# Kernel tuning notes

Hardware: AMD Instinct MI355X
Metric: run time of the kernel (lower is better)

## Reference

```python
import jax, jax.numpy as jnp
import numpy as np
from jax import lax

N = 20000        # nodes
E = 320000       # directed edges (avg degree 16)
F_IN = 512       # input feature dim
HID = 64         # hidden_layer
K_NEI = 8        # sampled neighbors per node
L = K_NEI + 1    # local subgraph size (self + neighbors)
N_TPL = 10       # N_templates
NT = 8           # N_templates_nodes
N_CLS = 6
ALPHA = 0.5      # FGW trade-off
EPS = 0.1        # entropic regularization
N_OUTER = 3      # outer CG iterations
N_SINK = 5       # sinkhorn iterations per outer step


def setup_inputs() -> dict:
    rng = np.random.default_rng(0)
    src = rng.integers(0, N, E).astype(np.int64)
    dst = rng.integers(0, N, E).astype(np.int64)
    edge_index = np.stack([src, dst])

    # fixed-size neighbor table (pad with self, mask)
    nbr = np.full((N, K_NEI), -1, np.int64)
    cnt = np.zeros(N, np.int64)
    for s, d in zip(src, dst):
        c = cnt[s]
        if c < K_NEI:
            nbr[s, c] = d
            cnt[s] = c + 1
    pad = nbr < 0
    self_col = np.arange(N, dtype=np.int64)
    nbr = np.where(pad, self_col[:, None], nbr)
    nbr_mask = np.concatenate([np.ones((N, 1)), (~pad).astype(np.float64)], 1).astype(np.float32)

    # local adjacency among {self, neighbors}: [N, L, L]
    idx_full = np.concatenate([self_col[:, None], nbr], 1)  # [N, L]
    edge_keys = np.unique(src * N + dst)
    keys = idx_full[:, :, None] * N + idx_full[:, None, :]
    C_local = np.isin(keys, edge_keys).astype(np.float32)

    ks = jax.random.split(jax.random.key(0), 10)
    x = jax.random.normal(ks[0], (N, F_IN), jnp.float32)
    W1 = jax.random.normal(ks[1], (F_IN, HID), jnp.float32) / np.float32(np.sqrt(F_IN))
    b1 = jnp.zeros((HID,), jnp.float32)
    W2 = jax.random.normal(ks[2], (HID, HID), jnp.float32) / np.float32(np.sqrt(HID))
    b2 = jnp.zeros((HID,), jnp.float32)
    t = jax.random.uniform(ks[3], (N_TPL, NT, NT), jnp.float32)
    templates = 0.5 * (t + jnp.swapaxes(t, 1, 2))  # symmetric template adjacency
    templates_features = jax.random.normal(ks[4], (N_TPL, NT, HID), jnp.float32)
    Wlin = jax.random.normal(ks[5], (HID + N_TPL, N_CLS), jnp.float32) / np.float32(np.sqrt(HID + N_TPL))
    blin = jnp.zeros((N_CLS,), jnp.float32)
    return {"x": x, "edge_index": jnp.asarray(edge_index), "nbr_idx": jnp.asarray(nbr),
            "nbr_mask": jnp.asarray(nbr_mask), "C_local": jnp.asarray(C_local),
            "W1": W1, "b1": b1, "W2": W2, "b2": b2,
            "templates": templates, "templates_features": templates_features,
            "Wlin": Wlin, "blin": blin}


def gcn(x, W, b, src, dst, n):
    xw = x @ W
    sl = jnp.arange(n)
    s = jnp.concatenate([src, sl])
    d = jnp.concatenate([dst, sl])
    deg = jax.ops.segment_sum(jnp.ones_like(s, jnp.float32), d, num_segments=n)
    dinv = lax.rsqrt(deg)
    coef = dinv[s] * dinv[d]
    return jax.ops.segment_sum(xw[s] * coef[:, None], d, num_segments=n) + b


def fgw_dist(M, C1, h1, C2, h2):
    # entropic fused GW (square loss) with fixed iterations; padded rows have h1 = 0
    f1 = C1 * C1
    f2 = C2 * C2
    constC = (f1 @ h1)[:, None] + (f2 @ h2)[None, :]
    T0 = h1[:, None] * h2[None, :]

    def outer(T, _):
        tens = constC - 2.0 * (C1 @ T @ C2)
        G = (1.0 - ALPHA) * M + ALPHA * tens
        Kmat = jnp.exp(-G / EPS)

        def sink(carry, _):
            u, v = carry
            u = h1 / (Kmat @ v + 1e-16)
            v = h2 / (Kmat.T @ u + 1e-16)
            return (u, v), None

        (u, v), _ = lax.scan(sink, (jnp.ones_like(h1), jnp.ones_like(h2)), None, length=N_SINK)
        return u[:, None] * Kmat * v[None, :], None

    T, _ = lax.scan(outer, T0, None, length=N_OUTER)
    tens = constC - 2.0 * (C1 @ T @ C2)
    return jnp.sum(T * ((1.0 - ALPHA) * M + ALPHA * tens))


def distance_to_template(x, nbr_idx, nbr_mask, C_local, templates_features, templates):
    n = x.shape[0]
    idx_full = jnp.concatenate([jnp.arange(n)[:, None], nbr_idx], axis=1)  # [N, L]
    xl = x[idx_full]  # [N, L, HID]
    # squared euclidean cost to each template: [N, T, L, NT]
    inner = jnp.einsum('nld,tmd->ntlm', xl, templates_features)
    M = (jnp.sum(xl * xl, -1)[:, None, :, None]
         + jnp.sum(templates_features * templates_features, -1)[None, :, None, :]
         - 2.0 * inner)
    h1 = nbr_mask / jnp.sum(nbr_mask, -1, keepdims=True)  # [N, L]
    h2 = jnp.full((NT,), 1.0 / NT, jnp.float32)

    per_tpl = jax.vmap(fgw_dist, in_axes=(0, None, None, 0, None))
    per_node = jax.vmap(per_tpl, in_axes=(0, 0, 0, None, None))
    return per_node(M, C_local, h1, templates, h2)  # [N, N_TPL]


def reference(x, edge_index, nbr_idx, nbr_mask, C_local, W1, b1, W2, b2,
              templates, templates_features, Wlin, blin):
    src, dst = edge_index[0], edge_index[1]
    n = x.shape[0]
    h = jax.nn.relu(gcn(x, W1, b1, src, dst, n))
    h = gcn(h, W2, b2, src, dst, n)
    y = distance_to_template(h, nbr_idx, nbr_mask, C_local, templates_features, templates)
    out = jnp.concatenate([h, y], axis=1) @ Wlin + blin
    return jax.nn.relu(out)
```

## Files before the change

kernel.cpp:

```cpp
#include <hip/hip_runtime.h>


#define NN   20000
#define EE   320000
#define FIN  512
#define HID  64
#define KNEI 8
#define LSZ  9
#define NTPL 10
#define NTN  8
#define NCLS 6
#define CAP  48

typedef unsigned short bf16_t;
typedef unsigned short us8 __attribute__((ext_vector_type(8)));

__device__ __forceinline__ float b2f(bf16_t u) {
  union { unsigned int i; float f; } v; v.i = ((unsigned int)u) << 16; return v.f;
}
__device__ __forceinline__ bf16_t f2b(float f) {
  union { float f; unsigned int i; } v; v.f = f;
  unsigned int x = v.i;
  return (bf16_t)((x + 0x7fffu + ((x >> 16) & 1u)) >> 16);
}
__device__ __forceinline__ float ldf(const void* p, long i, int fp32) {
  return fp32 ? ((const float*)p)[i] : b2f(((const bf16_t*)p)[i]);
}
__device__ __forceinline__ int ldi(const void* p, long i, int i64) {
  return i64 ? (int)((const long long*)p)[i] : ((const int*)p)[i];
}
__device__ __forceinline__ float frcp(float x) { return __builtin_amdgcn_rcpf(x); }

__global__ __launch_bounds__(128) void probe_kernel(const void* __restrict__ x,
                                                    const void* __restrict__ ei,
                                                    const void* __restrict__ tfeat,
                                                    int* __restrict__ flags,
                                                    float* __restrict__ tn2min) {
  __shared__ int sfl[2];
  __shared__ float tn2s[80];
  int tid = threadIdx.x;
  if (tid == 0) {
    int sane = 0;
    for (int k = 0; k < 64; k += 2) {
      bf16_t u = ((const bf16_t*)x)[k];
      int e = (u >> 7) & 0xff;
      if (e >= 112 && e <= 142) sane++;
    }
    int f0 = (sane < 24) ? 1 : 0;
    int zc = 0;
    for (int k = 1; k < 64; k += 2)
      if (((const int*)ei)[k] == 0) zc++;
    int f1 = (zc >= 16) ? 1 : 0;
    flags[0] = f0; flags[1] = f1;
    sfl[0] = f0; sfl[1] = f1;
  }
  __syncthreads();
  if (tid < 80) {
    int fF = sfl[0];
    float s = 0.f;
    for (int k = 0; k < HID; ++k) {
      float v = ldf(tfeat, (long)tid * HID + k, fF);
      s += v * v;
    }
    tn2s[tid] = s;
  }
  __syncthreads();
  if (tid == 0) {
    float gmin = 1e30f;
    for (int t = 0; t < NTPL; ++t) {
      float m = tn2s[t * 8];
      for (int r = 1; r < 8; ++r) m = fminf(m, tn2s[t * 8 + r]);
      tn2min[t] = m;
      gmin = fminf(gmin, m);
    }
    tn2min[NTPL] = gmin;
  }
}

__global__ __launch_bounds__(256) void hist_kernel(const void* __restrict__ ei,
                                                   int* __restrict__ cnt,
                                                   const int* __restrict__ flags) {
  int i = blockIdx.x * 256 + threadIdx.x;
  if (i < EE) atomicAdd(&cnt[ldi(ei, (long)EE + i, flags[1])], 1);
}
__global__ __launch_bounds__(256) void dinv_kernel(const int* __restrict__ cnt,
                                                   float* __restrict__ dinv) {
  int i = blockIdx.x * 256 + threadIdx.x;
  if (i < NN) dinv[i] = rsqrtf((float)cnt[i] + 1.0f);
}

__global__ __launch_bounds__(256) void scatter_kernel(const void* __restrict__ ei,
                                                      int* __restrict__ pos,
                                                      int* __restrict__ slot,
                                                      const int* __restrict__ flags) {
  int i = blockIdx.x * 256 + threadIdx.x;
  if (i >= EE) return;
  int i64 = flags[1];
  int s = ldi(ei, i, i64);
  int d = ldi(ei, (long)EE + i, i64);
  int p = atomicAdd(&pos[d], 1);
  if (p < CAP) slot[d * CAP + p] = s;
}

__global__ __launch_bounds__(256) void gemm1_kernel(const void* __restrict__ x,
                                                    const void* __restrict__ W1,
                                                    float* __restrict__ xw1,
                                                    const int* __restrict__ flags) {
  int wave = blockIdx.x * 4 + (threadIdx.x >> 6);
  int lane = threadIdx.x & 63;
  int row0 = wave * 4;
  if (row0 >= NN) return;
  float a0 = 0.f, a1 = 0.f, a2 = 0.f, a3 = 0.f;
  if (!flags[0]) {
    const bf16_t* xb = (const bf16_t*)x + (long)row0 * FIN;
    const bf16_t* wp = (const bf16_t*)W1;
#pragma unroll 2
    for (int k8 = 0; k8 < FIN / 8; ++k8) {
      us8 r0 = *(const us8*)(xb + k8 * 8);
      us8 r1 = *(const us8*)(xb + FIN + k8 * 8);
      us8 r2 = *(const us8*)(xb + 2 * FIN + k8 * 8);
      us8 r3 = *(const us8*)(xb + 3 * FIN + k8 * 8);
#pragma unroll
      for (int q = 0; q < 8; ++q) {
        float w = b2f(wp[(k8 * 8 + q) * HID + lane]);
        a0 += b2f(r0[q]) * w;
        a1 += b2f(r1[q]) * w;
        a2 += b2f(r2[q]) * w;
        a3 += b2f(r3[q]) * w;
      }
    }
  } else {
    const float* x0 = (const float*)x + (long)row0 * FIN;
    const float* wp = (const float*)W1;
#pragma unroll 8
    for (int k = 0; k < FIN; ++k) {
      float w = wp[k * HID + lane];
      a0 += x0[k] * w;
      a1 += x0[FIN + k] * w;
      a2 += x0[2 * FIN + k] * w;
      a3 += x0[3 * FIN + k] * w;
    }
  }
  xw1[(long)(row0 + 0) * HID + lane] = a0;
  xw1[(long)(row0 + 1) * HID + lane] = a1;
  xw1[(long)(row0 + 2) * HID + lane] = a2;
  xw1[(long)(row0 + 3) * HID + lane] = a3;
}

__global__ __launch_bounds__(256) void gemm2_kernel(const float* __restrict__ h,
                                                    const void* __restrict__ W2,
                                                    float* __restrict__ xw2,
                                                    const int* __restrict__ flags) {
  int wave = blockIdx.x * 4 + (threadIdx.x >> 6);
  int lane = threadIdx.x & 63;
  int row0 = wave * 4;
  if (row0 >= NN) return;
  int fF = flags[0];
  float a0 = 0.f, a1 = 0.f, a2 = 0.f, a3 = 0.f;
  const float* h0 = h + (long)row0 * HID;
#pragma unroll 4
  for (int k4 = 0; k4 < HID / 4; ++k4) {
    float4 r0 = *(const float4*)(h0 + k4 * 4);
    float4 r1 = *(const float4*)(h0 + HID + k4 * 4);
    float4 r2 = *(const float4*)(h0 + 2 * HID + k4 * 4);
    float4 r3 = *(const float4*)(h0 + 3 * HID + k4 * 4);
#pragma unroll
    for (int q = 0; q < 4; ++q) {
      float w = ldf(W2, (k4 * 4 + q) * HID + lane, fF);
      float e0 = (q == 0) ? r0.x : (q == 1) ? r0.y : (q == 2) ? r0.z : r0.w;
      float e1 = (q == 0) ? r1.x : (q == 1) ? r1.y : (q == 2) ? r1.z : r1.w;
      float e2 = (q == 0) ? r2.x : (q == 1) ? r2.y : (q == 2) ? r2.z : r2.w;
      float e3 = (q == 0) ? r3.x : (q == 1) ? r3.y : (q == 2) ? r3.z : r3.w;
      a0 += e0 * w; a1 += e1 * w; a2 += e2 * w; a3 += e3 * w;
    }
  }
  xw2[(long)(row0 + 0) * HID + lane] = a0;
  xw2[(long)(row0 + 1) * HID + lane] = a1;
  xw2[(long)(row0 + 2) * HID + lane] = a2;
  xw2[(long)(row0 + 3) * HID + lane] = a3;
}

__global__ __launch_bounds__(256) void gather_kernel(const float* __restrict__ xw,
                                                     const float* __restrict__ dinv,
                                                     const int* __restrict__ cnt,
                                                     const int* __restrict__ slot,
                                                     float* __restrict__ h,
                                                     const void* __restrict__ bias,
                                                     const int* __restrict__ flags,
                                                     int relu_bias) {
  int n = blockIdx.x * 4 + (threadIdx.x >> 6);
  if (n >= NN) return;
  int c = threadIdx.x & 63;
  float dn = dinv[n];
  float acc = xw[(long)n * HID + c] * dn;
  int m = cnt[n]; if (m > CAP) m = CAP;
  const int* sl = slot + (long)n * CAP;
  int sN = (m > 0) ? sl[0] : 0;
  for (int e = 0; e < m; ++e) {
    int s = sN;
    if (e + 1 < m) sN = sl[e + 1];
    acc += xw[(long)s * HID + c] * dinv[s];
  }
  acc *= dn;
  if (relu_bias) {
    acc += ldf(bias, c, flags[0]);
    acc = acc > 0.f ? acc : 0.f;
  }
  h[(long)n * HID + c] = acc;
}

__global__ __launch_bounds__(256) void norms_kernel(const float* __restrict__ h2,
                                                    const void* __restrict__ b2v,
                                                    float* __restrict__ n2,
                                                    const int* __restrict__ flags) {
  int n = blockIdx.x * 4 + (threadIdx.x >> 6);
  if (n >= NN) return;
  int c = threadIdx.x & 63;
  float v = h2[(long)n * HID + c] + ldf(b2v, c, flags[0]);
  float s = v * v;
  s += __shfl_xor(s, 1); s += __shfl_xor(s, 2); s += __shfl_xor(s, 4);
  s += __shfl_xor(s, 8); s += __shfl_xor(s, 16); s += __shfl_xor(s, 32);
  if (c == 0) n2[n] = s;
}

#define NODES_PB 4
#define TPN 80
#define XLP 65

__global__ __launch_bounds__(320, 2) void fgw_kernel(
    const float* __restrict__ h2,
    const void* __restrict__ b2v,
    const void* __restrict__ nbr_idx,
    const void* __restrict__ nbr_mask,
    const void* __restrict__ C_local,
    const void* __restrict__ tmpl,
    const void* __restrict__ tfeat,
    const void* __restrict__ Wlin,
    const void* __restrict__ blin,
    void* __restrict__ out,
    const int* __restrict__ flags,
    const float* __restrict__ tn2min,
    const float* __restrict__ n2)
{
  const int tid = threadIdx.x;
  const int fF = flags[0];
  const int fI = flags[1];
  const int nb = tid / TPN;
  const int local = tid - nb * TPN;
  const int t = local >> 3;
  const int j = local & 7;
  const int n = blockIdx.x * NODES_PB + nb;
  const int lane = tid & 63;
  const int ob = lane & 56;

  __shared__ float xlS[NODES_PB][LSZ][XLP];
  __shared__ float C1S[NODES_PB][81];
  __shared__ float hwS[NODES_PB][LSZ];
  __shared__ float f1S[NODES_PB][LSZ];
  __shared__ float xnS[NODES_PB][LSZ];
  __shared__ float distS[NODES_PB][NTPL];
  __shared__ float xmaxS[NODES_PB];
  __shared__ int   needS[NODES_PB];
  __shared__ int   sidxS[NODES_PB][LSZ];

  if (local < LSZ) {
    int idx = (local == 0) ? n : ldi(nbr_idx, (long)n * KNEI + local - 1, fI);
    sidxS[nb][local] = idx;
    xnS[nb][local] = n2[idx];
  }
  if (local < HID)
    xlS[nb][0][local] = h2[(long)n * HID + local] + ldf(b2v, local, fF);
  __syncthreads();

  if (local == 0) {
    float xm = xnS[nb][0];
#pragma unroll
    for (int l = 1; l < LSZ; ++l) xm = fmaxf(xm, xnS[nb][l]);
    xmaxS[nb] = xm;
    needS[nb] = ((sqrtf(tn2min[NTPL]) - sqrtf(xm)) >= 5.0990195f) ? 0 : 1;
  }
  __syncthreads();

  const int need = needS[nb];
  if (need) {
    for (int i = local; i < 8 * HID; i += TPN) {
      int l = 1 + (i >> 6), k = i & 63;
      xlS[nb][l][k] = h2[(long)sidxS[nb][l] * HID + k] + ldf(b2v, k, fF);
    }
    for (int i = local; i < 81; i += TPN)
      C1S[nb][i] = ldf(C_local, (long)n * 81 + i, fF);
  }
  __syncthreads();

  if (need && local < LSZ) {
    int l = local;
    float msum = 0.f, f1 = 0.f;
#pragma unroll
    for (int jj = 0; jj < LSZ; ++jj) {
      float mj = ldf(nbr_mask, (long)n * LSZ + jj, fF);
      msum += mj;
      float c = C1S[nb][l * LSZ + jj];
      f1 += c * c * mj;
    }
    float inv = frcp(msum);
    hwS[nb][l] = ldf(nbr_mask, (long)n * LSZ + l, fF) * inv;
    f1S[nb][l] = f1 * inv;
  }
  __syncthreads();

  bool slow = need && ((sqrtf(tn2min[t]) - sqrtf(xmaxS[nb])) < 5.0990195f);
  if (slow) {
    float C2c[NTN];
    float f2h2;
    {
      float s = 0.f;
#pragma unroll
      for (int m = 0; m < NTN; ++m) {
        C2c[m] = ldf(tmpl, t * 64 + m * 8 + j, fF);
        float r = ldf(tmpl, t * 64 + j * 8 + m, fF);
        s += r * r;
      }
      f2h2 = s * 0.125f;
    }
    float hwr[LSZ], f1r[LSZ];
#pragma unroll
    for (int l = 0; l < LSZ; ++l) { hwr[l] = hwS[nb][l]; f1r[l] = f1S[nb][l]; }

    float Mc[LSZ];
    {
      float accI[LSZ];
#pragma unroll
      for (int l = 0; l < LSZ; ++l) accI[l] = 0.f;
      float tn2 = 0.f;
      const long tb = (long)local * HID;
      for (int kb = 0; kb < 8; ++kb) {
        float r[8];
#pragma unroll
        for (int q = 0; q < 8; ++q) r[q] = ldf(tfeat, tb + kb * 8 + q, fF);
#pragma unroll
        for (int q = 0; q < 8; ++q) tn2 += r[q] * r[q];
#pragma unroll
        for (int l = 0; l < LSZ; ++l) {
          float s = 0.f;
#pragma unroll
          for (int q = 0; q < 8; ++q) s += xlS[nb][l][kb * 8 + q] * r[q];
          accI[l] += s;
        }
      }
#pragma unroll
      for (int l = 0; l < LSZ; ++l)
        Mc[l] = xnS[nb][l] + tn2 - 2.f * accI[l];
    }

    float Tc[LSZ], Kc[LSZ], u[LSZ];
#pragma unroll
    for (int l = 0; l < LSZ; ++l) Tc[l] = hwr[l] * 0.125f;

    float v = 1.0f;
    for (int outer = 0; outer < 3; ++outer) {
      float Ac[LSZ];
#pragma unroll
      for (int l = 0; l < LSZ; ++l) {
        float s = 0.f;
#pragma unroll
        for (int l2 = 0; l2 < LSZ; ++l2) s += C1S[nb][l * LSZ + l2] * Tc[l2];
        Ac[l] = s;
      }
#pragma unroll
      for (int l = 0; l < LSZ; ++l) {
        float s = 0.f;
#pragma unroll
        for (int m = 0; m < NTN; ++m) s += __shfl(Ac[l], ob + m) * C2c[m];
        float tens = f1r[l] + f2h2 - 2.f * s;
        Kc[l] = __expf(-5.0f * (Mc[l] + tens));
      }
      v = 1.0f;
      for (int it = 0; it < 5; ++it) {
#pragma unroll
        for (int l = 0; l < LSZ; ++l) {
          float p = Kc[l] * v;
          p += __shfl_xor(p, 1); p += __shfl_xor(p, 2); p += __shfl_xor(p, 4);
          u[l] = hwr[l] * frcp(p + 1e-16f);
        }
        float s = 0.f;
#pragma unroll
        for (int l = 0; l < LSZ; ++l) s += Kc[l] * u[l];
        v = 0.125f * frcp(s + 1e-16f);
      }
#pragma unroll
      for (int l = 0; l < LSZ; ++l) Tc[l] = u[l] * Kc[l] * v;
    }
    {
      float Ac[LSZ];
#pragma unroll
      for (int l = 0; l < LSZ; ++l) {
        float s = 0.f;
#pragma unroll
        for (int l2 = 0; l2 < LSZ; ++l2) s += C1S[nb][l * LSZ + l2] * Tc[l2];
        Ac[l] = s;
      }
      float cl = 0.f;
#pragma unroll
      for (int l = 0; l < LSZ; ++l) {
        float s = 0.f;
#pragma unroll
        for (int m = 0; m < NTN; ++m) s += __shfl(Ac[l], ob + m) * C2c[m];
        float tens = f1r[l] + f2h2 - 2.f * s;
        cl += Tc[l] * 0.5f * (Mc[l] + tens);
      }
      cl += __shfl_xor(cl, 1); cl += __shfl_xor(cl, 2); cl += __shfl_xor(cl, 4);
      if (j == 0) distS[nb][t] = cl;
    }
  } else if (j == 0) {
    distS[nb][t] = 0.f;
  }
  __syncthreads();

  if (local < NCLS) {
    int c = local;
    float acc = ldf(blin, c, fF);
#pragma unroll
    for (int k = 0; k < HID; ++k)
      acc += xlS[nb][0][k] * ldf(Wlin, k * NCLS + c, fF);
#pragma unroll
    for (int tt = 0; tt < NTPL; ++tt)
      acc += distS[nb][tt] * ldf(Wlin, (HID + tt) * NCLS + c, fF);
    float r = acc > 0.f ? acc : 0.f;
    if (fF) ((float*)out)[(long)n * NCLS + c] = r;
    else    ((bf16_t*)out)[(long)n * NCLS + c] = f2b(r);
  }
}

extern "C" void kernel_launch(void* const* d_in, const int* in_sizes, int n_in,
                              void* d_out, int out_size, void* d_ws, size_t ws_size,
                              hipStream_t stream) {
  (void)in_sizes; (void)n_in; (void)out_size; (void)ws_size;
  const void* x     = d_in[0];
  const void* ei    = d_in[1];
  const void* nbr   = d_in[2];
  const void* nmask = d_in[3];
  const void* Cl    = d_in[4];
  const void* W1    = d_in[5];
  const void* b1    = d_in[6];
  const void* W2    = d_in[7];
  const void* b2    = d_in[8];
  const void* tmpl  = d_in[9];
  const void* tfeat = d_in[10];
  const void* Wlin  = d_in[11];
  const void* blin  = d_in[12];

  int*   flags  = (int*)d_ws;
  float* tn2min = (float*)d_ws + 4;
  float* dinv   = (float*)d_ws + 16;
  float* n2     = dinv + NN;
  int*   cnt    = (int*)(n2 + NN);
  int*   pos    = cnt + NN;
  int*   slot   = pos + NN;
  float* bufA   = (float*)(slot + (long)CAP * NN);
  float* bufB   = bufA + (long)NN * HID;

  probe_kernel<<<1, 128, 0, stream>>>(x, ei, tfeat, flags, tn2min);

  hipMemsetAsync(cnt, 0, NN * sizeof(int), stream);
  hipMemsetAsync(pos, 0, NN * sizeof(int), stream);
  hist_kernel<<<(EE + 255) / 256, 256, 0, stream>>>(ei, cnt, flags);
  dinv_kernel<<<(NN + 255) / 256, 256, 0, stream>>>(cnt, dinv);
  scatter_kernel<<<(EE + 255) / 256, 256, 0, stream>>>(ei, pos, slot, flags);

  gemm1_kernel<<<NN / 16, 256, 0, stream>>>(x, W1, bufA, flags);
  gather_kernel<<<NN / 4, 256, 0, stream>>>(bufA, dinv, cnt, slot, bufB,
                                            b1, flags, 1);
  gemm2_kernel<<<NN / 16, 256, 0, stream>>>(bufB, W2, bufA, flags);
  gather_kernel<<<NN / 4, 256, 0, stream>>>(bufA, dinv, cnt, slot, bufB,
                                            b2, flags, 0);

  norms_kernel<<<NN / 4, 256, 0, stream>>>(bufB, b2, n2, flags);

  fgw_kernel<<<NN / NODES_PB, 320, 0, stream>>>(bufB, b2, nbr, nmask, Cl, tmpl,
                                                tfeat, Wlin, blin, d_out, flags,
                                                tn2min, n2);
}
```

Baseline: 343.0 us.

## Fuse GCN degree, second GEMM and norms into gather kernels; stage Wlin in LDS

Drops the separate histogram and dinv kernels and reuses the scatter position counter as the in-degree, recomputing rsqrt of the degree inline. The first gather is fused with the 64x64 W2 GEMM through wave shuffles, and the second gather is fused with the squared-norm computation. Slot indices are read as int4 with two accumulators. The final linear layer's weights are staged in shared memory inside the FGW kernel. This cuts launches and intermediate global traffic, at the cost of extra per-edge rsqrt and cnt loads and a per-block Wlin copy.

```diff
diff --git a/kernel.cpp b/kernel.cpp
--- a/kernel.cpp
+++ b/kernel.cpp
@@ -75,18 +75,6 @@
     }
     tn2min[NTPL] = gmin;
   }
-}
-
-__global__ __launch_bounds__(256) void hist_kernel(const void* __restrict__ ei,
-                                                   int* __restrict__ cnt,
-                                                   const int* __restrict__ flags) {
-  int i = blockIdx.x * 256 + threadIdx.x;
-  if (i < EE) atomicAdd(&cnt[ldi(ei, (long)EE + i, flags[1])], 1);
-}
-__global__ __launch_bounds__(256) void dinv_kernel(const int* __restrict__ cnt,
-                                                   float* __restrict__ dinv) {
-  int i = blockIdx.x * 256 + threadIdx.x;
-  if (i < NN) dinv[i] = rsqrtf((float)cnt[i] + 1.0f);
 }
 
 __global__ __launch_bounds__(256) void scatter_kernel(const void* __restrict__ ei,
@@ -147,76 +135,74 @@
   xw1[(long)(row0 + 3) * HID + lane] = a3;
 }
 
-__global__ __launch_bounds__(256) void gemm2_kernel(const float* __restrict__ h,
-                                                    const void* __restrict__ W2,
-                                                    float* __restrict__ xw2,
-                                                    const int* __restrict__ flags) {
-  int wave = blockIdx.x * 4 + (threadIdx.x >> 6);
-  int lane = threadIdx.x & 63;
-  int row0 = wave * 4;
-  if (row0 >= NN) return;
+__global__ __launch_bounds__(256) void gatherA_kernel(const float* __restrict__ xw,
+                                                      const int* __restrict__ cnt,
+                                                      const int* __restrict__ slot,
+                                                      float* __restrict__ xw2,
+                                                      const void* __restrict__ b1v,
+                                                      const void* __restrict__ W2,
+                                                      const int* __restrict__ flags) {
+  int n = blockIdx.x * 4 + (threadIdx.x >> 6);
+  if (n >= NN) return;
   int fF = flags[0];
-  float a0 = 0.f, a1 = 0.f, a2 = 0.f, a3 = 0.f;
-  const float* h0 = h + (long)row0 * HID;
-#pragma unroll 4
-  for (int k4 = 0; k4 < HID / 4; ++k4) {
-    float4 r0 = *(const float4*)(h0 + k4 * 4);
-    float4 r1 = *(const float4*)(h0 + HID + k4 * 4);
-    float4 r2 = *(const float4*)(h0 + 2 * HID + k4 * 4);
-    float4 r3 = *(const float4*)(h0 + 3 * HID + k4 * 4);
-#pragma unroll
-    for (int q = 0; q < 4; ++q) {
-      float w = ldf(W2, (k4 * 4 + q) * HID + lane, fF);
-      float e0 = (q == 0) ? r0.x : (q == 1) ? r0.y : (q == 2) ? r0.z : r0.w;
-      float e1 = (q == 0) ? r1.x : (q == 1) ? r1.y : (q == 2) ? r1.z : r1.w;
-      float e2 = (q == 0) ? r2.x : (q == 1) ? r2.y : (q == 2) ? r2.z : r2.w;
-      float e3 = (q == 0) ? r3.x : (q == 1) ? r3.y : (q == 2) ? r3.z : r3.w;
-      a0 += e0 * w; a1 += e1 * w; a2 += e2 * w; a3 += e3 * w;
-    }
-  }
-  xw2[(long)(row0 + 0) * HID + lane] = a0;
-  xw2[(long)(row0 + 1) * HID + lane] = a1;
-  xw2[(long)(row0 + 2) * HID + lane] = a2;
-  xw2[(long)(row0 + 3) * HID + lane] = a3;
-}
-
-__global__ __launch_bounds__(256) void gather_kernel(const float* __restrict__ xw,
-                                                     const float* __restrict__ dinv,
-                                                     const int* __restrict__ cnt,
-                                                     const int* __restrict__ slot,
-                                                     float* __restrict__ h,
-                                                     const void* __restrict__ bias,
-                                                     const int* __restrict__ flags,
-                                                     int relu_bias) {
+  int c = threadIdx.x & 63;
+  float dn = rsqrtf((float)cnt[n] + 1.0f);
+  float acc = xw[(long)n * HID + c] * dn;
+  int m = cnt[n]; if (m > CAP) m = CAP;
+  const int* sl = slot + (long)n * CAP;
+  float accB = 0.f;
+  for (int e0 = 0; e0 < m; e0 += 8) {
+    int4 sa = *(const int4*)(sl + e0);
+    int4 sb = *(const int4*)(sl + e0 + 4);
+    if (e0 + 0 < m) acc  += xw[(long)sa.x * HID + c] * rsqrtf((float)cnt[sa.x] + 1.0f);
+    if (e0 + 1 < m) accB += xw[(long)sa.y * HID + c] * rsqrtf((float)cnt[sa.y] + 1.0f);
+    if (e0 + 2 < m) acc  += xw[(long)sa.z * HID + c] * rsqrtf((float)cnt[sa.z] + 1.0f);
+    if (e0 + 3 < m) accB += xw[(long)sa.w * HID + c] * rsqrtf((float)cnt[sa.w] + 1.0f);
+    if (e0 + 4 < m) acc  += xw[(long)sb.x * HID + c] * rsqrtf((float)cnt[sb.x] + 1.0f);
+    if (e0 + 5 < m) accB += xw[(long)sb.y * HID + c] * rsqrtf((float)cnt[sb.y] + 1.0f);
+    if (e0 + 6 < m) acc  += xw[(long)sb.z * HID + c] * rsqrtf((float)cnt[sb.z] + 1.0f);
+    if (e0 + 7 < m) accB += xw[(long)sb.w * HID + c] * rsqrtf((float)cnt[sb.w] + 1.0f);
+  }
+  float h1 = (acc + accB) * dn + ldf(b1v, c, fF);
+  h1 = h1 > 0.f ? h1 : 0.f;
+
+  float o = 0.f;
+#pragma unroll 8
+  for (int k = 0; k < HID; ++k)
+    o += __shfl(h1, k) * ldf(W2, k * HID + c, fF);
+  xw2[(long)n * HID + c] = o;
+}
+
+__global__ __launch_bounds__(256) void gatherB_kernel(const float* __restrict__ xw,
+                                                      const int* __restrict__ cnt,
+                                                      const int* __restrict__ slot,
+                                                      float* __restrict__ h,
+                                                      float* __restrict__ n2,
+                                                      const void* __restrict__ b2v,
+                                                      const int* __restrict__ flags) {
   int n = blockIdx.x * 4 + (threadIdx.x >> 6);
   if (n >= NN) return;
   int c = threadIdx.x & 63;
-  float dn = dinv[n];
+  float dn = rsqrtf((float)cnt[n] + 1.0f);
   float acc = xw[(long)n * HID + c] * dn;
   int m = cnt[n]; if (m > CAP) m = CAP;
   const int* sl = slot + (long)n * CAP;
-  int sN = (m > 0) ? sl[0] : 0;
-  for (int e = 0; e < m; ++e) {
-    int s = sN;
-    if (e + 1 < m) sN = sl[e + 1];
-    acc += xw[(long)s * HID + c] * dinv[s];
-  }
-  acc *= dn;
-  if (relu_bias) {
-    acc += ldf(bias, c, flags[0]);
-    acc = acc > 0.f ? acc : 0.f;
-  }
+  float accB = 0.f;
+  for (int e0 = 0; e0 < m; e0 += 8) {
+    int4 sa = *(const int4*)(sl + e0);
+    int4 sb = *(const int4*)(sl + e0 + 4);
+    if (e0 + 0 < m) acc  += xw[(long)sa.x * HID + c] * rsqrtf((float)cnt[sa.x] + 1.0f);
+    if (e0 + 1 < m) accB += xw[(long)sa.y * HID + c] * rsqrtf((float)cnt[sa.y] + 1.0f);
+    if (e0 + 2 < m) acc  += xw[(long)sa.z * HID + c] * rsqrtf((float)cnt[sa.z] + 1.0f);
+    if (e0 + 3 < m) accB += xw[(long)sa.w * HID + c] * rsqrtf((float)cnt[sa.w] + 1.0f);
+    if (e0 + 4 < m) acc  += xw[(long)sb.x * HID + c] * rsqrtf((float)cnt[sb.x] + 1.0f);
+    if (e0 + 5 < m) accB += xw[(long)sb.y * HID + c] * rsqrtf((float)cnt[sb.y] + 1.0f);
+    if (e0 + 6 < m) acc  += xw[(long)sb.z * HID + c] * rsqrtf((float)cnt[sb.z] + 1.0f);
+    if (e0 + 7 < m) accB += xw[(long)sb.w * HID + c] * rsqrtf((float)cnt[sb.w] + 1.0f);
+  }
+  acc = (acc + accB) * dn;
   h[(long)n * HID + c] = acc;
-}
-
-__global__ __launch_bounds__(256) void norms_kernel(const float* __restrict__ h2,
-                                                    const void* __restrict__ b2v,
-                                                    float* __restrict__ n2,
-                                                    const int* __restrict__ flags) {
-  int n = blockIdx.x * 4 + (threadIdx.x >> 6);
-  if (n >= NN) return;
-  int c = threadIdx.x & 63;
-  float v = h2[(long)n * HID + c] + ldf(b2v, c, flags[0]);
+  float v = acc + ldf(b2v, c, flags[0]);
   float s = v * v;
   s += __shfl_xor(s, 1); s += __shfl_xor(s, 2); s += __shfl_xor(s, 4);
   s += __shfl_xor(s, 8); s += __shfl_xor(s, 16); s += __shfl_xor(s, 32);
@@ -262,6 +248,11 @@
   __shared__ float xmaxS[NODES_PB];
   __shared__ int   needS[NODES_PB];
   __shared__ int   sidxS[NODES_PB][LSZ];
+  __shared__ float WlinS[(HID + NTPL) * NCLS + NCLS];
+
+  for (int i = tid; i < (HID + NTPL) * NCLS; i += 320)
+    WlinS[i] = ldf(Wlin, i, fF);
+  if (tid < NCLS) WlinS[(HID + NTPL) * NCLS + tid] = ldf(blin, tid, fF);
 
   if (local < LSZ) {
     int idx = (local == 0) ? n : ldi(nbr_idx, (long)n * KNEI + local - 1, fI);
@@ -418,13 +409,13 @@
 
   if (local < NCLS) {
     int c = local;
-    float acc = ldf(blin, c, fF);
+    float acc = WlinS[(HID + NTPL) * NCLS + c];
 #pragma unroll
     for (int k = 0; k < HID; ++k)
-      acc += xlS[nb][0][k] * ldf(Wlin, k * NCLS + c, fF);
+      acc += xlS[nb][0][k] * WlinS[k * NCLS + c];
 #pragma unroll
     for (int tt = 0; tt < NTPL; ++tt)
-      acc += distS[nb][tt] * ldf(Wlin, (HID + tt) * NCLS + c, fF);
+      acc += distS[nb][tt] * WlinS[(HID + tt) * NCLS + c];
     float r = acc > 0.f ? acc : 0.f;
     if (fF) ((float*)out)[(long)n * NCLS + c] = r;
     else    ((bf16_t*)out)[(long)n * NCLS + c] = f2b(r);
@@ -451,32 +442,22 @@
 
   int*   flags  = (int*)d_ws;
   float* tn2min = (float*)d_ws + 4;
-  float* dinv   = (float*)d_ws + 16;
-  float* n2     = dinv + NN;
-  int*   cnt    = (int*)(n2 + NN);
-  int*   pos    = cnt + NN;
+  float* n2     = (float*)d_ws + 16;
+  int*   pos    = (int*)(n2 + NN);
   int*   slot   = pos + NN;
   float* bufA   = (float*)(slot + (long)CAP * NN);
   float* bufB   = bufA + (long)NN * HID;
 
   probe_kernel<<<1, 128, 0, stream>>>(x, ei, tfeat, flags, tn2min);
 
-  hipMemsetAsync(cnt, 0, NN * sizeof(int), stream);
   hipMemsetAsync(pos, 0, NN * sizeof(int), stream);
-  hist_kernel<<<(EE + 255) / 256, 256, 0, stream>>>(ei, cnt, flags);
-  dinv_kernel<<<(NN + 255) / 256, 256, 0, stream>>>(cnt, dinv);
   scatter_kernel<<<(EE + 255) / 256, 256, 0, stream>>>(ei, pos, slot, flags);
 
   gemm1_kernel<<<NN / 16, 256, 0, stream>>>(x, W1, bufA, flags);
-  gather_kernel<<<NN / 4, 256, 0, stream>>>(bufA, dinv, cnt, slot, bufB,
-                                            b1, flags, 1);
-  gemm2_kernel<<<NN / 16, 256, 0, stream>>>(bufB, W2, bufA, flags);
-  gather_kernel<<<NN / 4, 256, 0, stream>>>(bufA, dinv, cnt, slot, bufB,
-                                            b2, flags, 0);
-
-  norms_kernel<<<NN / 4, 256, 0, stream>>>(bufB, b2, n2, flags);
-
-  fgw_kernel<<<NN / NODES_PB, 320, 0, stream>>>(bufB, b2, nbr, nmask, Cl, tmpl,
+  gatherA_kernel<<<NN / 4, 256, 0, stream>>>(bufA, pos, slot, bufB, b1, W2, flags);
+  gatherB_kernel<<<NN / 4, 256, 0, stream>>>(bufB, pos, slot, bufA, n2, b2, flags);
+
+  fgw_kernel<<<NN / NODES_PB, 320, 0, stream>>>(bufA, b2, nbr, nmask, Cl, tmpl,
                                                 tfeat, Wlin, blin, d_out, flags,
                                                 tn2min, n2);
 }
```

After: 317.1 us. 7.6% less time.
